# Optimization experiments

Hardware: AMD Instinct MI355X
Metric: run time of the kernel (lower is better)

The kernel has to match this reference:

```python
import jax, jax.numpy as jnp
import numpy as np

P = 8  # patch size (fixed in module)


def setup_inputs() -> dict:
    key = jax.random.key(0)
    k0, k1, k2, k3 = jax.random.split(key, 4)
    d, B, H, W = 64, 4, 256, 256
    x = jax.random.normal(k0, (B, d, H, W), dtype=jnp.float32)
    # conv weights (bias=False). 1x1 convs stored as [out, in]; depthwise as [out,1,3,3]
    w1 = jax.random.normal(k1, (6 * d, d), dtype=jnp.float32) * 0.05
    w_dw = jax.random.normal(k2, (6 * d, 1, 3, 3), dtype=jnp.float32) * 0.1
    w_out = jax.random.normal(k3, (d, 2 * d), dtype=jnp.float32) * 0.05
    ln_w = jnp.ones((2 * d,), dtype=jnp.float32)
    ln_b = jnp.zeros((2 * d,), dtype=jnp.float32)
    return {"x": x, "w1": w1, "w_dw": w_dw, "w_out": w_out, "ln_w": ln_w, "ln_b": ln_b}


def _to_patches(t):
    # [b,c,H,W] -> [b,c,H/P,W/P,P,P]
    b, c, h, w = t.shape
    return t.reshape(b, c, h // P, P, w // P, P).transpose(0, 1, 2, 4, 3, 5)


def reference(x, w1, w_dw, w_out, ln_w, ln_b):
    B, C, H, W = x.shape
    # to_hidden: 1x1 conv, dim -> 6*dim
    hidden = jnp.einsum('bchw,oc->bohw', x, w1)
    # to_hidden_dw: depthwise 3x3, groups = 6*dim
    hidden = jax.lax.conv_general_dilated(
        hidden, w_dw, window_strides=(1, 1), padding='SAME',
        feature_group_count=w_dw.shape[0],
        dimension_numbers=('NCHW', 'OIHW', 'NCHW'))
    q, k, v = jnp.split(hidden, 3, axis=1)  # each [B, 2C, H, W]
    # patch-wise frequency-domain correlation: irfft2(rfft2(q) * rfft2(k))
    qf = jnp.fft.rfft2(_to_patches(q))
    kf = jnp.fft.rfft2(_to_patches(k))
    out = jnp.fft.irfft2(qf * kf, s=(P, P))  # [B,2C,H/P,W/P,P,P]
    b, c = out.shape[:2]
    out = out.transpose(0, 1, 2, 4, 3, 5).reshape(b, c, H, W)
    # LayerNorm (WithBias) over the channel dim, eps=1e-5, biased variance
    mu = out.mean(axis=1, keepdims=True)
    var = out.var(axis=1, keepdims=True)
    out = (out - mu) / jnp.sqrt(var + 1e-5) * ln_w[None, :, None, None] + ln_b[None, :, None, None]
    # gate by v, then project_out: 1x1 conv, 2*dim -> dim
    out = v * out
    return jnp.einsum('bchw,oc->bohw', out, w_out)
```

## Files before the change

kernel.cpp:

```cpp
#include <hip/hip_runtime.h>

#define NTHREADS 512

#define NB   4
#define HH   256
#define WW   256

#define XF     0
#define HIDA   0
#define Q_U    8192
#define K_U    17408
#define CST    72
#define CORRU  0
#define REDU   8192
#define BFRU   8192
#define MU_U   26624
#define RS_U   26752
#define SMEM_U 26880

typedef short s16x8 __attribute__((ext_vector_type(8)));
typedef float f32x16 __attribute__((ext_vector_type(16)));
typedef _Float16 h16x8 __attribute__((ext_vector_type(8)));
typedef _Float16 h16x4 __attribute__((ext_vector_type(4)));
typedef _Float16 h16x2 __attribute__((ext_vector_type(2)));

__device__ inline unsigned short f2bf(float f) {
    unsigned u = __builtin_bit_cast(unsigned, f);
    u += 0x7FFFu + ((u >> 16) & 1u);
    return (unsigned short)(u >> 16);
}
__device__ inline float bf2f(unsigned short s) {
    return __builtin_bit_cast(float, (unsigned)s << 16);
}
__device__ inline unsigned short f2h(float f) {
    _Float16 h = (_Float16)f;
    return __builtin_bit_cast(unsigned short, h);
}

__device__ inline float fdot2(unsigned a, unsigned b, float c) {
#if __has_builtin(__builtin_amdgcn_fdot2)
    return __builtin_amdgcn_fdot2(__builtin_bit_cast(h16x2, a),
                                  __builtin_bit_cast(h16x2, b), c, false);
#else
    h16x2 av = __builtin_bit_cast(h16x2, a);
    h16x2 bv = __builtin_bit_cast(h16x2, b);
    return c + (float)av[0] * (float)bv[0] + (float)av[1] * (float)bv[1];
#endif
}

__global__ __launch_bounds__(256)
void fsas_prepack(const float* __restrict__ w1, const float* __restrict__ wout,
                  unsigned short* __restrict__ ws)
{
    int t = blockIdx.x * 256 + threadIdx.x;
    if (t < 24576) {
        int b = t & 7, ln = (t >> 3) & 63, ks = (t >> 9) & 3, mtc = t >> 11;
        int l32 = ln & 31, half = ln >> 5;
        int o = mtc * 32 + l32;
        int kk = ks * 16 + half * 8 + b;
        ws[t] = f2bf(w1[o * 64 + kk]);
    } else if (t < 40960) {
        int idx = t - 24576;
        int lo = idx >= 8192;
        if (lo) idx -= 8192;
        int b = idx & 7, ln = (idx >> 3) & 63, ks = (idx >> 9) & 7, mtp = idx >> 12;
        int l32 = ln & 31, half = ln >> 5;
        int o = mtp * 32 + l32;
        int kk = ks * 16 + half * 8 + b;
        float v = wout[o * 128 + kk];
        unsigned short hi = f2bf(v);
        ws[t] = lo ? f2bf(v - bf2f(hi)) : hi;
    }
}

__global__ __launch_bounds__(NTHREADS, 4)
void fsas_fused(const float* __restrict__ x,
                const float* __restrict__ wdw,
                const unsigned short* __restrict__ wsu,
                const float* __restrict__ lnw,
                const float* __restrict__ lnb,
                float* __restrict__ out)
{
    __shared__ unsigned short su[SMEM_U];

    const int tid = threadIdx.x;
    const int wv  = tid >> 6;
    const int ln  = tid & 63;
    const int l32 = ln & 31, half = ln >> 5;
    const int lin  = (blockIdx.z * 32 + blockIdx.y) * 32 + blockIdx.x;
    const int orig = (lin & 7) * 512 + (lin >> 3);
    const int pw = orig & 31;
    const int ph = (orig >> 5) & 31;
    const int b  = orig >> 10;
    const int h0  = ph * 8;
    const int w0  = pw * 8;

    for (int it = 0; it < 2; ++it) {
        int u = tid + it * NTHREADS;
        int pos = u & 127, grp = u >> 7;
        uint4 o4 = {0u, 0u, 0u, 0u};
        if (pos < 100) {
            int r = pos / 10, q = pos - r * 10;
            int h = h0 - 1 + r, w = w0 - 1 + q;
            if ((unsigned)h < (unsigned)HH && (unsigned)w < (unsigned)WW) {
                const float* xp = x + ((size_t)(b * 64 + grp * 8) * HH + h) * WW + w;
                unsigned pk[4];
#pragma unroll
                for (int k = 0; k < 4; ++k) {
                    float v0 = xp[(2 * k)     * (HH * WW)];
                    float v1 = xp[(2 * k + 1) * (HH * WW)];
                    pk[k] = (unsigned)f2bf(v0) | ((unsigned)f2bf(v1) << 16);
                }
                o4.x = pk[0]; o4.y = pk[1]; o4.z = pk[2]; o4.w = pk[3];
            }
        }
        int lane = (pos & 31) + 32 * (grp & 1);
        int nt = pos >> 5, ks = grp >> 1;
        *(uint4*)(su + XF + ((nt * 4 + ks) * 64 + lane) * 8) = o4;
    }
    __syncthreads();

    const s16x8* waf = (const s16x8*)wsu;
    const int mt2 = wv & 1, nt = (wv >> 1) & 3;
    const int pos = nt * 32 + l32;
    const int r10 = pos / 10, c10 = pos - r10 * 10;
    const int posoff = r10 * 12 + c10;
    const bool pvalid = pos < 100;

    s16x8 breg[4];
#pragma unroll
    for (int ks = 0; ks < 4; ++ks)
        breg[ks] = *(const s16x8*)(su + XF + ((nt * 4 + ks) * 64 + ln) * 8);
    __syncthreads();

    uint4 vA, vB;
    const int dw_oc = tid >> 3, dw_py = tid & 7;

#pragma unroll
    for (int rnd = 0; rnd < 6; ++rnd) {
        {
            int mtc = rnd * 2 + mt2;
            f32x16 acc = {};
#pragma unroll
            for (int ks = 0; ks < 4; ++ks) {
                s16x8 afr = waf[(mtc * 4 + ks) * 64 + ln];
                acc = __builtin_amdgcn_mfma_f32_32x32x16_bf16(afr, breg[ks], acc, 0, 0, 0);
            }
            if (pvalid) {
#pragma unroll
                for (int rr = 0; rr < 16; ++rr) {
                    int o_l = mt2 * 32 + (rr & 3) + 8 * (rr >> 2) + 4 * half;
                    su[HIDA + o_l * 120 + posoff] = f2h(acc[rr]);
                }
            }
        }
        __syncthreads();
        {
            int oc = dw_oc, py = dw_py;
            const float* wr = wdw + (rnd * 64 + oc) * 9;
            unsigned w01[3], w2z[3];
#pragma unroll
            for (int r3 = 0; r3 < 3; ++r3) {
                w01[r3] = (unsigned)f2h(wr[3 * r3]) | ((unsigned)f2h(wr[3 * r3 + 1]) << 16);
                w2z[r3] = (unsigned)f2h(wr[3 * r3 + 2]);
            }
            const unsigned short* hb = su + HIDA + oc * 120 + py * 12;
            float o_[8] = {0.f,0.f,0.f,0.f,0.f,0.f,0.f,0.f};
#pragma unroll
            for (int r3 = 0; r3 < 3; ++r3) {
                uint2 ua = *(const uint2*)(hb + r3 * 12);
                uint2 ub = *(const uint2*)(hb + r3 * 12 + 4);
                uint2 uc = *(const uint2*)(hb + r3 * 12 + 8);
                unsigned W[6] = {ua.x, ua.y, ub.x, ub.y, uc.x, uc.y};
                unsigned A[5];
#pragma unroll
                for (int k = 0; k < 5; ++k)
                    A[k] = __builtin_amdgcn_alignbit(W[k + 1], W[k], 16);
#pragma unroll
                for (int px = 0; px < 8; px += 2) {
                    int m = px >> 1;
                    o_[px]     = fdot2(w01[r3], W[m], fdot2(w2z[r3], W[m + 1], o_[px]));
                    o_[px + 1] = fdot2(w01[r3], A[m], fdot2(w2z[r3], A[m + 1], o_[px + 1]));
                }
            }
            uint4 o4;
            o4.x = (unsigned)f2h(o_[0]) | ((unsigned)f2h(o_[1]) << 16);
            o4.y = (unsigned)f2h(o_[2]) | ((unsigned)f2h(o_[3]) << 16);
            o4.z = (unsigned)f2h(o_[4]) | ((unsigned)f2h(o_[5]) << 16);
            o4.w = (unsigned)f2h(o_[6]) | ((unsigned)f2h(o_[7]) << 16);
            if (rnd < 4) {
                int buf = rnd >> 1;
                int cb  = (rnd & 1) * 64 + oc;
                int cs  = cb & 7;
                *(uint4*)(su + Q_U + buf * 9216 + cb * CST + ((py ^ cs) * 8)) = o4;
            } else if (rnd == 4) {
                vA = o4;
            } else {
                vB = o4;
            }
        }
        if (rnd < 5) __syncthreads();
    }
    __syncthreads();

    {
        int oc = dw_oc, py = dw_py;
#pragma unroll
        for (int cc = 0; cc < 2; ++cc) {
            int c = oc + cc * 64, cs = c & 7;
            const unsigned short* qr = su + Q_U + c * CST;
            const unsigned short* kr = su + K_U + c * CST;
            float o0[8] = {0.f,0.f,0.f,0.f,0.f,0.f,0.f,0.f};
#pragma unroll
            for (int a = 0; a < 8; ++a) {
                uint4 uq = *(const uint4*)(qr + ((a ^ cs) * 8));
                int k0 = (py - a) & 7;
                uint4 uk = *(const uint4*)(kr + ((k0 ^ cs) * 8));
                unsigned qw[4] = {uq.x, uq.y, uq.z, uq.w};
                unsigned kw[4] = {uk.x, uk.y, uk.z, uk.w};
                unsigned kr0[8];
#pragma unroll
                for (int p = 0; p < 4; ++p) {
                    kr0[2 * p]     = __builtin_amdgcn_perm(kw[(p + 3) & 3], kw[p], 0x07060100u);
                    kr0[2 * p + 1] = __builtin_amdgcn_alignbit(kw[p], kw[p], 16);
                }
#pragma unroll
                for (int j = 0; j < 8; ++j) {
#pragma unroll
                    for (int p = 0; p < 4; ++p)
                        o0[j] = fdot2(qw[p], kr0[(j - 2 * p) & 7], o0[j]);
                }
            }
            uint4 a4;
            a4.x = (unsigned)f2h(o0[0]) | ((unsigned)f2h(o0[1]) << 16);
            a4.y = (unsigned)f2h(o0[2]) | ((unsigned)f2h(o0[3]) << 16);
            a4.z = (unsigned)f2h(o0[4]) | ((unsigned)f2h(o0[5]) << 16);
            a4.w = (unsigned)f2h(o0[6]) | ((unsigned)f2h(o0[7]) << 16);
            *(uint4*)(su + CORRU + c * 64 + ((py ^ cs) * 8)) = a4;
        }
    }
    __syncthreads();

    {
        float* redF = (float*)(su + REDU);
        int px = tid & 63, grp = tid >> 6;
        int prow = px >> 3, pcol = px & 7;
        float s = 0.f, s2 = 0.f;
#pragma unroll
        for (int i = 0; i < 16; ++i) {
            int c = i * 8 + grp;
            float v = (float)__builtin_bit_cast(_Float16,
                        su[CORRU + c * 64 + ((prow ^ (c & 7)) * 8) + pcol]);
            s += v; s2 += v * v;
        }
        redF[grp * 64 + px] = s;
        redF[512 + grp * 64 + px] = s2;
    }
    __syncthreads();
    if (tid < 64) {
        float* redF = (float*)(su + REDU);
        float s = 0.f, s2 = 0.f;
#pragma unroll
        for (int g = 0; g < 8; ++g) {
            s  += redF[g * 64 + tid];
            s2 += redF[512 + g * 64 + tid];
        }
        float m = s * (1.f / 128.f);
        float var = s2 * (1.f / 128.f) - m * m;
        ((float*)(su + MU_U))[tid] = m;
        ((float*)(su + RS_U))[tid] = rsqrtf(var + 1e-5f);
    }
    __syncthreads();

    {
        int oc = dw_oc, py = dw_py;
        const float* muF = (const float*)(su + MU_U);
        const float* rsF = (const float*)(su + RS_U);
        float4 m0 = *(const float4*)(muF + py * 8);
        float4 m1 = *(const float4*)(muF + py * 8 + 4);
        float4 r0 = *(const float4*)(rsF + py * 8);
        float4 r1 = *(const float4*)(rsF + py * 8 + 4);
        float mm[8] = {m0.x, m0.y, m0.z, m0.w, m1.x, m1.y, m1.z, m1.w};
        float rr[8] = {r0.x, r0.y, r0.z, r0.w, r1.x, r1.y, r1.z, r1.w};
#pragma unroll
        for (int cc = 0; cc < 2; ++cc) {
            int c = oc + cc * 64, cs = c & 7;
            uint4 cu = *(const uint4*)(su + CORRU + c * 64 + ((py ^ cs) * 8));
            h16x8 ch = __builtin_bit_cast(h16x8, cu);
            h16x8 vh = __builtin_bit_cast(h16x8, cc ? vB : vA);
            float wc = lnw[c], bc = lnb[c];
            int base = BFRU + (((py >> 2) * 8 + (c >> 4)) * 64 + 8 * (py & 3) + 32 * ((c >> 3) & 1)) * 8 + (c & 7);
#pragma unroll
            for (int j = 0; j < 8; ++j) {
                float t = (((float)ch[j] - mm[j]) * rr[j] * wc + bc) * (float)vh[j];
                su[base + j * 8] = f2bf(t);
            }
        }
    }
    __syncthreads();

    if (wv < 4) {
        int mtp = wv & 1, ntp = wv >> 1;
        const s16x8* whi = (const s16x8*)(wsu + 24576);
        const s16x8* wlo = (const s16x8*)(wsu + 32768);
        f32x16 acc = {};
#pragma unroll
        for (int ks = 0; ks < 8; ++ks) {
            s16x8 bfr = *(const s16x8*)(su + BFRU + ((ntp * 8 + ks) * 64 + ln) * 8);
            s16x8 ah  = whi[(mtp * 8 + ks) * 64 + ln];
            acc = __builtin_amdgcn_mfma_f32_32x32x16_bf16(ah, bfr, acc, 0, 0, 0);
            s16x8 al  = wlo[(mtp * 8 + ks) * 64 + ln];
            acc = __builtin_amdgcn_mfma_f32_32x32x16_bf16(al, bfr, acc, 0, 0, 0);
        }
        int px = ntp * 32 + l32;
        int py = px >> 3, wx = px & 7;
#pragma unroll
        for (int r = 0; r < 16; ++r) {
            int row = (r >> 2) * 8 + half * 4 + (r & 3);
            int o = mtp * 32 + row;
            out[(((size_t)(b * 64 + o) * HH) + h0 + py) * WW + w0 + wx] = acc[r];
        }
    }
}

extern "C" void kernel_launch(void* const* d_in, const int* in_sizes, int n_in,
                              void* d_out, int out_size, void* d_ws, size_t ws_size,
                              hipStream_t stream) {
    const float* x    = (const float*)d_in[0];
    const float* w1   = (const float*)d_in[1];
    const float* wdw  = (const float*)d_in[2];
    const float* wout = (const float*)d_in[3];
    const float* lnw  = (const float*)d_in[4];
    const float* lnb  = (const float*)d_in[5];
    float* o = (float*)d_out;
    unsigned short* ws = (unsigned short*)d_ws;

    fsas_prepack<<<160, 256, 0, stream>>>(w1, wout, ws);
    dim3 grid(32, 32, NB);
    fsas_fused<<<grid, dim3(NTHREADS), 0, stream>>>(x, wdw, ws, lnw, lnb, o);
}
```

Before: 276.3 us.

## Double-buffer hidden tile, hoist depthwise weights, prepermute K in LDS

Alternates the 1x1-conv output between two LDS buffers so one of the two barriers per round can be dropped. Loads and packs all six rounds of depthwise weights into registers once at kernel start. Stores K already permuted into its rotated pairs so the correlation loop skips the per-iteration perm and alignbit work. This raises LDS use and register pressure, which can reduce occupancy, and it trims the padded edge-column read in the depthwise step.

```diff
diff --git a/kernel.cpp b/kernel.cpp
--- a/kernel.cpp
+++ b/kernel.cpp
@@ -9,14 +9,14 @@
 #define XF     0
 #define HIDA   0
 #define Q_U    8192
-#define K_U    17408
-#define CST    72
+#define KP_U   16384
+#define HIDB   32768
 #define CORRU  0
 #define REDU   8192
 #define BFRU   8192
-#define MU_U   26624
-#define RS_U   26752
-#define SMEM_U 26880
+#define MU_U   40448
+#define RS_U   40576
+#define SMEM_U 40704
 
 typedef short s16x8 __attribute__((ext_vector_type(8)));
 typedef float f32x16 __attribute__((ext_vector_type(16)));
@@ -95,6 +95,19 @@
     const int h0  = ph * 8;
     const int w0  = pw * 8;
 
+    const int dw_oc = tid >> 3, dw_py = tid & 7;
+
+    unsigned w01[6][3], w2z[6][3];
+#pragma unroll
+    for (int rnd = 0; rnd < 6; ++rnd) {
+        const float* wr = wdw + (rnd * 64 + dw_oc) * 9;
+#pragma unroll
+        for (int r3 = 0; r3 < 3; ++r3) {
+            w01[rnd][r3] = (unsigned)f2h(wr[3 * r3]) | ((unsigned)f2h(wr[3 * r3 + 1]) << 16);
+            w2z[rnd][r3] = (unsigned)f2h(wr[3 * r3 + 2]);
+        }
+    }
+
     for (int it = 0; it < 2; ++it) {
         int u = tid + it * NTHREADS;
         int pos = u & 127, grp = u >> 7;
@@ -134,10 +147,10 @@
     __syncthreads();
 
     uint4 vA, vB;
-    const int dw_oc = tid >> 3, dw_py = tid & 7;
 
 #pragma unroll
     for (int rnd = 0; rnd < 6; ++rnd) {
+        const int hid_base = (rnd & 1) ? HIDB : HIDA;
         {
             int mtc = rnd * 2 + mt2;
             f32x16 acc = {};
@@ -150,37 +163,31 @@
 #pragma unroll
                 for (int rr = 0; rr < 16; ++rr) {
                     int o_l = mt2 * 32 + (rr & 3) + 8 * (rr >> 2) + 4 * half;
-                    su[HIDA + o_l * 120 + posoff] = f2h(acc[rr]);
+                    su[hid_base + o_l * 120 + posoff] = f2h(acc[rr]);
                 }
             }
         }
         __syncthreads();
         {
             int oc = dw_oc, py = dw_py;
-            const float* wr = wdw + (rnd * 64 + oc) * 9;
-            unsigned w01[3], w2z[3];
-#pragma unroll
-            for (int r3 = 0; r3 < 3; ++r3) {
-                w01[r3] = (unsigned)f2h(wr[3 * r3]) | ((unsigned)f2h(wr[3 * r3 + 1]) << 16);
-                w2z[r3] = (unsigned)f2h(wr[3 * r3 + 2]);
-            }
-            const unsigned short* hb = su + HIDA + oc * 120 + py * 12;
+            const unsigned short* hb = su + hid_base + oc * 120 + py * 12;
             float o_[8] = {0.f,0.f,0.f,0.f,0.f,0.f,0.f,0.f};
 #pragma unroll
             for (int r3 = 0; r3 < 3; ++r3) {
                 uint2 ua = *(const uint2*)(hb + r3 * 12);
                 uint2 ub = *(const uint2*)(hb + r3 * 12 + 4);
                 uint2 uc = *(const uint2*)(hb + r3 * 12 + 8);
-                unsigned W[6] = {ua.x, ua.y, ub.x, ub.y, uc.x, uc.y};
+                unsigned W[5] = {ua.x, ua.y, ub.x, ub.y, uc.x};
                 unsigned A[5];
 #pragma unroll
-                for (int k = 0; k < 5; ++k)
+                for (int k = 0; k < 4; ++k)
                     A[k] = __builtin_amdgcn_alignbit(W[k + 1], W[k], 16);
+                A[4] = __builtin_amdgcn_alignbit(W[4], W[4], 16);
 #pragma unroll
                 for (int px = 0; px < 8; px += 2) {
                     int m = px >> 1;
-                    o_[px]     = fdot2(w01[r3], W[m], fdot2(w2z[r3], W[m + 1], o_[px]));
-                    o_[px + 1] = fdot2(w01[r3], A[m], fdot2(w2z[r3], A[m + 1], o_[px + 1]));
+                    o_[px]     = fdot2(w01[rnd][r3], W[m], fdot2(w2z[rnd][r3], W[m + 1], o_[px]));
+                    o_[px + 1] = fdot2(w01[rnd][r3], A[m], fdot2(w2z[rnd][r3], A[m + 1], o_[px + 1]));
                 }
             }
             uint4 o4;
@@ -188,18 +195,30 @@
             o4.y = (unsigned)f2h(o_[2]) | ((unsigned)f2h(o_[3]) << 16);
             o4.z = (unsigned)f2h(o_[4]) | ((unsigned)f2h(o_[5]) << 16);
             o4.w = (unsigned)f2h(o_[6]) | ((unsigned)f2h(o_[7]) << 16);
-            if (rnd < 4) {
-                int buf = rnd >> 1;
-                int cb  = (rnd & 1) * 64 + oc;
-                int cs  = cb & 7;
-                *(uint4*)(su + Q_U + buf * 9216 + cb * CST + ((py ^ cs) * 8)) = o4;
+            int cb = (rnd & 1) * 64 + oc;
+            int cs = cb & 7;
+            if (rnd < 2) {
+                *(uint4*)(su + Q_U + cb * 64 + ((py ^ cs) * 8)) = o4;
+            } else if (rnd < 4) {
+                unsigned kw[4] = {o4.x, o4.y, o4.z, o4.w};
+                uint4 p0, p1;
+                p0.x = __builtin_amdgcn_perm(kw[3], kw[0], 0x07060100u);
+                p0.y = __builtin_amdgcn_alignbit(kw[0], kw[0], 16);
+                p0.z = __builtin_amdgcn_perm(kw[0], kw[1], 0x07060100u);
+                p0.w = __builtin_amdgcn_alignbit(kw[1], kw[1], 16);
+                p1.x = __builtin_amdgcn_perm(kw[1], kw[2], 0x07060100u);
+                p1.y = __builtin_amdgcn_alignbit(kw[2], kw[2], 16);
+                p1.z = __builtin_amdgcn_perm(kw[2], kw[3], 0x07060100u);
+                p1.w = __builtin_amdgcn_alignbit(kw[3], kw[3], 16);
+                unsigned short* kd = su + KP_U + cb * 128 + ((py ^ cs) * 16);
+                *(uint4*)kd = p0;
+                *(uint4*)(kd + 8) = p1;
             } else if (rnd == 4) {
                 vA = o4;
             } else {
                 vB = o4;
             }
         }
-        if (rnd < 5) __syncthreads();
     }
     __syncthreads();
 
@@ -208,27 +227,23 @@
 #pragma unroll
         for (int cc = 0; cc < 2; ++cc) {
             int c = oc + cc * 64, cs = c & 7;
-            const unsigned short* qr = su + Q_U + c * CST;
-            const unsigned short* kr = su + K_U + c * CST;
+            const unsigned short* qr = su + Q_U  + c * 64;
+            const unsigned short* kr = su + KP_U + c * 128;
             float o0[8] = {0.f,0.f,0.f,0.f,0.f,0.f,0.f,0.f};
 #pragma unroll
             for (int a = 0; a < 8; ++a) {
                 uint4 uq = *(const uint4*)(qr + ((a ^ cs) * 8));
                 int k0 = (py - a) & 7;
-                uint4 uk = *(const uint4*)(kr + ((k0 ^ cs) * 8));
+                const unsigned short* kpr = kr + ((k0 ^ cs) * 16);
+                uint4 uk0 = *(const uint4*)(kpr);
+                uint4 uk1 = *(const uint4*)(kpr + 8);
                 unsigned qw[4] = {uq.x, uq.y, uq.z, uq.w};
-                unsigned kw[4] = {uk.x, uk.y, uk.z, uk.w};
-                unsigned kr0[8];
-#pragma unroll
-                for (int p = 0; p < 4; ++p) {
-                    kr0[2 * p]     = __builtin_amdgcn_perm(kw[(p + 3) & 3], kw[p], 0x07060100u);
-                    kr0[2 * p + 1] = __builtin_amdgcn_alignbit(kw[p], kw[p], 16);
-                }
+                unsigned kp[8] = {uk0.x, uk0.y, uk0.z, uk0.w, uk1.x, uk1.y, uk1.z, uk1.w};
 #pragma unroll
                 for (int j = 0; j < 8; ++j) {
 #pragma unroll
                     for (int p = 0; p < 4; ++p)
-                        o0[j] = fdot2(qw[p], kr0[(j - 2 * p) & 7], o0[j]);
+                        o0[j] = fdot2(qw[p], kp[(j - 2 * p) & 7], o0[j]);
                 }
             }
             uint4 a4;
```

After: 260.1 us. 1.06x faster.
